# Kernel optimization log

Measured on AMD Instinct MI355X. Metric: run time of the kernel, lower is better.

Reference implementation:

```python
import jax, jax.numpy as jnp
import numpy as np

FP8_MAX = 448.0  # float8_e4m3fn max
BLOCK = 128

def act_quant(x, block_size=BLOCK):
    """Block-wise fp8 quantization along the last dim.
    Returns (q, scale): q has x.shape in float8_e4m3fn, scale has shape
    x.shape[:-1] + (K // block_size,).
    """
    *lead, K = x.shape
    nb = K // block_size
    xb = x.reshape(*lead, nb, block_size)
    amax = jnp.max(jnp.abs(xb), axis=-1)                # (..., nb)
    scale = jnp.maximum(amax / FP8_MAX, 1e-12)
    q = (xb / scale[..., None]).astype(jnp.float8_e4m3fn).reshape(x.shape)
    return q, scale

def fp8_gemm_optimized(xq, xs, kq, ks, block_size=BLOCK):
    """Dequant-scaled GEMM. xq:[M,K] fp8, xs:[M,K/bs]; kq:[K,N] fp8, ks:[K,N/bs]."""
    M, K = xq.shape
    Kk, N = kq.shape
    kb, nb = K // block_size, N // block_size
    # dequantize with per-block scales
    xd = (xq.astype(jnp.float32).reshape(M, kb, block_size)
          * xs[:, :, None]).reshape(M, K)
    kd = (kq.astype(jnp.float32).reshape(K, nb, block_size)
          * ks[:, :, None]).reshape(K, N)
    return xd @ kd

def setup_inputs() -> dict:
    key = jax.random.key(0)
    k1, k2, k3 = jax.random.split(key, 3)
    M, K, N = 16384, 4096, 4096
    x = jax.random.normal(k1, (M, K), dtype=jnp.float32)
    # lecun_normal: std = 1/sqrt(fan_in)
    kernel = jax.random.normal(k2, (K, N), dtype=jnp.float32) / jnp.sqrt(jnp.float32(K))
    bias = jnp.zeros((N,), dtype=jnp.float32)
    return {"x": x, "kernel": kernel, "bias": bias}

def reference(x, kernel, bias):
    xq, xs = act_quant(x, BLOCK)
    kq, ks = act_quant(kernel, BLOCK)
    y = fp8_gemm_optimized(xq, xs, kq, ks, BLOCK)
    return y + bias
```

## Files before the change

kernel.cpp:

```cpp
#include <hip/hip_runtime.h>


typedef __attribute__((ext_vector_type(8))) short short8;
typedef __attribute__((ext_vector_type(4))) float f32x4;
typedef unsigned short ushort_t;

__device__ __forceinline__ float fp8_round_trip(float v) {
    int p = __builtin_amdgcn_cvt_pk_fp8_f32(v, v, 0, false);
    return __builtin_amdgcn_cvt_f32_fp8(p, 0);
}

__device__ __forceinline__ ushort_t f32_to_bf16(float f) {
    union { float f; unsigned u; } un; un.f = f;
    unsigned r = un.u + 0x7fffu + ((un.u >> 16) & 1u);
    return (ushort_t)(r >> 16);
}

__device__ __forceinline__ void async16(const void* g, void* l) {
    __builtin_amdgcn_global_load_lds(
        (const __attribute__((address_space(1))) unsigned int*)g,
        (__attribute__((address_space(3))) unsigned int*)l,
        16, 0, 0);
}

__global__ __launch_bounds__(256) void quant_x_kernel(
        const float* __restrict__ x, ushort_t* __restrict__ xd) {
    size_t tid  = (size_t)blockIdx.x * 256 + threadIdx.x;
    size_t base = tid * 4;
    float4 v = *(const float4*)(x + base);
    float amax = fmaxf(fmaxf(fabsf(v.x), fabsf(v.y)),
                       fmaxf(fabsf(v.z), fabsf(v.w)));
    #pragma unroll
    for (int m = 1; m < 32; m <<= 1)
        amax = fmaxf(amax, __shfl_xor(amax, m, 64));
    float scale = fmaxf(amax / 448.0f, 1e-12f);
    ushort4 o;
    o.x = f32_to_bf16(fp8_round_trip(v.x / scale) * scale);
    o.y = f32_to_bf16(fp8_round_trip(v.y / scale) * scale);
    o.z = f32_to_bf16(fp8_round_trip(v.z / scale) * scale);
    o.w = f32_to_bf16(fp8_round_trip(v.w / scale) * scale);
    *(ushort4*)(xd + base) = o;
}

__global__ __launch_bounds__(256) void quant_w_kernel(
        const float* __restrict__ w, ushort_t* __restrict__ bt,
        int K, int N) {
    __shared__ float lds[128 * 65];
    int k0 = blockIdx.x * 64;
    int n0 = blockIdx.y * 128;
    int t = threadIdx.x;
    int wid = t >> 6, lane = t & 63;
    int half = lane >> 5, l32 = lane & 31;

    #pragma unroll
    for (int rr = 0; rr < 8; ++rr) {
        int klocal = wid * 16 + rr * 2 + half;
        int k = k0 + klocal;
        float4 v = *(const float4*)(w + (size_t)k * N + n0 + l32 * 4);
        float amax = fmaxf(fmaxf(fabsf(v.x), fabsf(v.y)),
                           fmaxf(fabsf(v.z), fabsf(v.w)));
        #pragma unroll
        for (int m = 1; m < 32; m <<= 1)
            amax = fmaxf(amax, __shfl_xor(amax, m, 64));
        float scale = fmaxf(amax / 448.0f, 1e-12f);
        int nl = l32 * 4;
        lds[(nl + 0) * 65 + klocal] = fp8_round_trip(v.x / scale) * scale;
        lds[(nl + 1) * 65 + klocal] = fp8_round_trip(v.y / scale) * scale;
        lds[(nl + 2) * 65 + klocal] = fp8_round_trip(v.z / scale) * scale;
        lds[(nl + 3) * 65 + klocal] = fp8_round_trip(v.w / scale) * scale;
    }
    __syncthreads();
    #pragma unroll
    for (int it = 0; it < 8; ++it) {
        int idx = it * 256 + t;
        int j = idx >> 4;
        int c = idx & 15;
        const float* p = &lds[j * 65 + c * 4];
        ushort4 o;
        o.x = f32_to_bf16(p[0]);
        o.y = f32_to_bf16(p[1]);
        o.z = f32_to_bf16(p[2]);
        o.w = f32_to_bf16(p[3]);
        *(ushort4*)(bt + (size_t)(n0 + j) * K + k0 + c * 4) = o;
    }
}


#define GBAR()    asm volatile("s_barrier" ::: "memory")
#define WAITL(n)  asm volatile("s_waitcnt lgkmcnt(" #n ")" ::: "memory")
#define WAITV(n)  asm volatile("s_waitcnt vmcnt(" #n ")" ::: "memory")

#define STAGE_A(h, kt, buf) do {                                             \
    const ushort_t* g_ = aSrc + (size_t)((h) * 128) * K + (size_t)(kt) * 64; \
    ushort_t* l_ = &sm[buf][0][(h) * 8192] + wid * 512;                      \
    async16(g_, l_);                                                         \
    async16(g_ + (size_t)64 * K, l_ + 4096);                                 \
} while (0)

#define STAGE_B(h, kt, buf) do {                                             \
    const ushort_t* g_ = bSrc + (size_t)((h) * 128) * K + (size_t)(kt) * 64; \
    ushort_t* l_ = &sm[buf][1][(h) * 8192] + wid * 512;                      \
    async16(g_, l_);                                                         \
    async16(g_ + (size_t)64 * K, l_ + 4096);                                 \
} while (0)

#define LDA_(dst, buf, hsel) do {                                            \
    const char* p_ = smA[buf] + aOff + (hsel) * 8192;                        \
    _Pragma("unroll") for (int m_ = 0; m_ < 4; ++m_) {                       \
        dst[m_][0] = *(const short8*)(p_ + m_ * 2048);                       \
        dst[m_][1] = *(const short8*)(p_ + m_ * 2048 + 64);                  \
    }                                                                        \
} while (0)

#define LDB_(buf, nsel) do {                                                 \
    const char* p_ = smB[buf] + bOff + (nsel) * 4096;                        \
    _Pragma("unroll") for (int n_ = 0; n_ < 2; ++n_) {                       \
        bb[n_][0] = *(const short8*)(p_ + n_ * 2048);                        \
        bb[n_][1] = *(const short8*)(p_ + n_ * 2048 + 64);                   \
    }                                                                        \
} while (0)

#define MFMAQ(AS, mb, nb) do {                                               \
    _Pragma("unroll") for (int m_ = 0; m_ < 4; ++m_)                         \
    _Pragma("unroll") for (int n_ = 0; n_ < 2; ++n_) {                       \
        acc[(mb) + m_][(nb) + n_] = __builtin_amdgcn_mfma_f32_16x16x32_bf16( \
            AS[m_][0], bb[n_][0], acc[(mb) + m_][(nb) + n_], 0, 0, 0);       \
        acc[(mb) + m_][(nb) + n_] = __builtin_amdgcn_mfma_f32_16x16x32_bf16( \
            AS[m_][1], bb[n_][1], acc[(mb) + m_][(nb) + n_], 0, 0, 0);       \
    }                                                                        \
} while (0)

#define PH_TOP()  GBAR(); WAITL(0); __builtin_amdgcn_sched_barrier(0);       \
                  __builtin_amdgcn_s_setprio(1)
#define PH_END()  __builtin_amdgcn_s_setprio(0); GBAR()

__global__ __launch_bounds__(512, 2) void gemm256_kernel(
        const ushort_t* __restrict__ A, const ushort_t* __restrict__ B,
        const float* __restrict__ bias, float* __restrict__ C,
        int M, int N, int K) {
    __shared__ ushort_t sm[2][2][16384];

    const int t = threadIdx.x;
    const int wid = t >> 6;
    const int lane = t & 63;
    const int quad = lane >> 4, l16 = lane & 15;
    const int wr = wid >> 2, wcn = wid & 3;

    const int nwg = gridDim.x;
    const int bid = blockIdx.x;
    int wg = bid;
    if ((nwg & 7) == 0) { const int cpx = nwg >> 3; wg = (bid & 7) * cpx + (bid >> 3); }
    const int nbn = N >> 8;
    const int bm = wg / nbn, bn = wg % nbn;

    const int srow = t >> 3;
    const int scol = ((((t & 7) * 16) ^ (((t >> 5) & 1) << 5)) >> 1);
    const ushort_t* aSrc = A + (size_t)(bm * 256 + srow) * K + scol;
    const ushort_t* bSrc = B + (size_t)(bn * 256 + srow) * K + scol;

    const int xr = ((l16 >> 2) & 1) << 5;
    const int tbase = l16 * 128 + ((quad * 16) ^ xr);
    const int aOff = wr * 16384 + tbase;
    const int bOff = wcn * 8192 + tbase;
    const char* smA[2] = { (const char*)sm[0][0], (const char*)sm[1][0] };
    const char* smB[2] = { (const char*)sm[0][1], (const char*)sm[1][1] };

    f32x4 acc[8][4] = {};
    short8 a0[4][2], a1[4][2], bb[2][2];

    const int NT = K >> 6;
    const int NI = NT >> 1;

    STAGE_A(0, 0, 0); STAGE_A(1, 0, 0); STAGE_B(0, 0, 0); STAGE_B(1, 0, 0);
    STAGE_A(0, 1, 1); STAGE_A(1, 1, 1); STAGE_B(0, 1, 1);
    WAITV(6); GBAR();

    for (int i = 0; i < NI; ++i) {
        const int T  = 2 * i;
        const int t1 = T + 1;
        const int t2 = (T + 2 < NT) ? T + 2 : 0;
        const int t3 = (T + 3 < NT) ? T + 3 : 0;

        LDB_(0, 0); LDA_(a0, 0, 0);
        STAGE_B(1, t1, 1);
        WAITL(8);
        PH_TOP(); MFMAQ(a0, 0, 0); PH_END();
        LDA_(a1, 0, 1);
        PH_TOP(); MFMAQ(a1, 4, 0); PH_END();
        LDB_(0, 1);
        STAGE_A(0, t2, 0);
        PH_TOP(); MFMAQ(a0, 0, 2); PH_END();
        STAGE_A(1, t2, 0);
        WAITV(4);
        GBAR(); __builtin_amdgcn_s_setprio(1); MFMAQ(a1, 4, 2); PH_END();
        LDB_(1, 0); LDA_(a0, 1, 0);
        STAGE_B(0, t2, 0);
        WAITL(8);
        PH_TOP(); MFMAQ(a0, 0, 0); PH_END();
        LDA_(a1, 1, 1);
        STAGE_B(1, t2, 0);
        PH_TOP(); MFMAQ(a1, 4, 0); PH_END();
        LDB_(1, 1);
        STAGE_A(0, t3, 1);
        PH_TOP(); MFMAQ(a0, 0, 2); PH_END();
        STAGE_A(1, t3, 1);
        STAGE_B(0, t3, 1);
        WAITV(6);
        GBAR(); __builtin_amdgcn_s_setprio(1); MFMAQ(a1, 4, 2); PH_END();
    }

    #pragma unroll
    for (int nt = 0; nt < 4; ++nt) {
        const int col = bn * 256 + wcn * 64 + nt * 16 + l16;
        const float bv = bias[col];
        #pragma unroll
        for (int mt = 0; mt < 8; ++mt) {
            const int row0 = bm * 256 + wr * 128 + mt * 16 + quad * 4;
            #pragma unroll
            for (int r = 0; r < 4; ++r)
                C[(size_t)(row0 + r) * N + col] = acc[mt][nt][r] + bv;
        }
    }
}

extern "C" void kernel_launch(void* const* d_in, const int* in_sizes, int n_in,
                              void* d_out, int out_size, void* d_ws, size_t ws_size,
                              hipStream_t stream) {
    const float* x    = (const float*)d_in[0];
    const float* w    = (const float*)d_in[1];
    const float* bias = (const float*)d_in[2];
    float* out = (float*)d_out;

    const int N = in_sizes[2];
    const int K = in_sizes[1] / N;
    const int M = in_sizes[0] / K;

    ushort_t* xd = (ushort_t*)d_ws;
    ushort_t* bt = xd + (size_t)M * K;

    quant_x_kernel<<<(size_t)M * K / 1024, 256, 0, stream>>>(x, xd);
    quant_w_kernel<<<dim3(K / 64, N / 128), 256, 0, stream>>>(w, bt, K, N);
    gemm256_kernel<<<dim3((M / 256) * (N / 256)), 512, 0, stream>>>(
        xd, bt, bias, out, M, N, K);
}
```

Baseline: 954.5 us.

## Widen LDS XOR swizzle to 8-way and double per-thread work in x quantization

The GEMM's LDS tile swizzle changes from a single-bit XOR (one 32-byte toggle) to a 3-bit row-dependent XOR over 16-byte chunks. The async global-to-LDS staging columns and the short8 fragment reads are updated to match, with the aim of removing LDS bank conflicts on the MFMA operand loads. The x quantization kernel now has each thread process two float4 groups from two 128-element blocks, halving the grid and giving more memory-level parallelism per thread. The swizzle has to stay consistent between writer and reader; a mismatch would produce wrong results, not just slower ones.

```diff
diff --git a/kernel.cpp b/kernel.cpp
--- a/kernel.cpp
+++ b/kernel.cpp
@@ -26,20 +26,34 @@
 __global__ __launch_bounds__(256) void quant_x_kernel(
         const float* __restrict__ x, ushort_t* __restrict__ xd) {
     size_t tid  = (size_t)blockIdx.x * 256 + threadIdx.x;
-    size_t base = tid * 4;
-    float4 v = *(const float4*)(x + base);
-    float amax = fmaxf(fmaxf(fabsf(v.x), fabsf(v.y)),
-                       fmaxf(fabsf(v.z), fabsf(v.w)));
-    #pragma unroll
-    for (int m = 1; m < 32; m <<= 1)
-        amax = fmaxf(amax, __shfl_xor(amax, m, 64));
-    float scale = fmaxf(amax / 448.0f, 1e-12f);
-    ushort4 o;
-    o.x = f32_to_bf16(fp8_round_trip(v.x / scale) * scale);
-    o.y = f32_to_bf16(fp8_round_trip(v.y / scale) * scale);
-    o.z = f32_to_bf16(fp8_round_trip(v.z / scale) * scale);
-    o.w = f32_to_bf16(fp8_round_trip(v.w / scale) * scale);
-    *(ushort4*)(xd + base) = o;
+    int lane = threadIdx.x & 63;
+    size_t wbase = (tid >> 6) * 512;
+    size_t i0 = wbase + (size_t)lane * 4;
+    size_t i1 = i0 + 256;
+    float4 v0 = *(const float4*)(x + i0);
+    float4 v1 = *(const float4*)(x + i1);
+    float a0 = fmaxf(fmaxf(fabsf(v0.x), fabsf(v0.y)),
+                     fmaxf(fabsf(v0.z), fabsf(v0.w)));
+    float a1 = fmaxf(fmaxf(fabsf(v1.x), fabsf(v1.y)),
+                     fmaxf(fabsf(v1.z), fabsf(v1.w)));
+    #pragma unroll
+    for (int m = 1; m < 32; m <<= 1) {
+        a0 = fmaxf(a0, __shfl_xor(a0, m, 64));
+        a1 = fmaxf(a1, __shfl_xor(a1, m, 64));
+    }
+    float s0 = fmaxf(a0 / 448.0f, 1e-12f);
+    float s1 = fmaxf(a1 / 448.0f, 1e-12f);
+    ushort4 o0, o1;
+    o0.x = f32_to_bf16(fp8_round_trip(v0.x / s0) * s0);
+    o0.y = f32_to_bf16(fp8_round_trip(v0.y / s0) * s0);
+    o0.z = f32_to_bf16(fp8_round_trip(v0.z / s0) * s0);
+    o0.w = f32_to_bf16(fp8_round_trip(v0.w / s0) * s0);
+    o1.x = f32_to_bf16(fp8_round_trip(v1.x / s1) * s1);
+    o1.y = f32_to_bf16(fp8_round_trip(v1.y / s1) * s1);
+    o1.z = f32_to_bf16(fp8_round_trip(v1.z / s1) * s1);
+    o1.w = f32_to_bf16(fp8_round_trip(v1.w / s1) * s1);
+    *(ushort4*)(xd + i0) = o0;
+    *(ushort4*)(xd + i1) = o1;
 }
 
 __global__ __launch_bounds__(256) void quant_w_kernel(
@@ -105,18 +119,18 @@
 } while (0)
 
 #define LDA_(dst, buf, hsel) do {                                            \
-    const char* p_ = smA[buf] + aOff + (hsel) * 8192;                        \
+    const char* p_ = smA[buf] + aBase + (hsel) * 8192;                       \
     _Pragma("unroll") for (int m_ = 0; m_ < 4; ++m_) {                       \
-        dst[m_][0] = *(const short8*)(p_ + m_ * 2048);                       \
-        dst[m_][1] = *(const short8*)(p_ + m_ * 2048 + 64);                  \
+        dst[m_][0] = *(const short8*)(p_ + m_ * 2048 + cs0);                 \
+        dst[m_][1] = *(const short8*)(p_ + m_ * 2048 + cs1);                 \
     }                                                                        \
 } while (0)
 
 #define LDB_(buf, nsel) do {                                                 \
-    const char* p_ = smB[buf] + bOff + (nsel) * 4096;                        \
+    const char* p_ = smB[buf] + bBase + (nsel) * 4096;                       \
     _Pragma("unroll") for (int n_ = 0; n_ < 2; ++n_) {                       \
-        bb[n_][0] = *(const short8*)(p_ + n_ * 2048);                        \
-        bb[n_][1] = *(const short8*)(p_ + n_ * 2048 + 64);                   \
+        bb[n_][0] = *(const short8*)(p_ + n_ * 2048 + cs0);                  \
+        bb[n_][1] = *(const short8*)(p_ + n_ * 2048 + cs1);                  \
     }                                                                        \
 } while (0)
 
@@ -154,14 +168,15 @@
     const int bm = wg / nbn, bn = wg % nbn;
 
     const int srow = t >> 3;
-    const int scol = ((((t & 7) * 16) ^ (((t >> 5) & 1) << 5)) >> 1);
+    const int scol = ((((t & 7) * 16) ^ (((t >> 3) & 7) << 4)) >> 1);
     const ushort_t* aSrc = A + (size_t)(bm * 256 + srow) * K + scol;
     const ushort_t* bSrc = B + (size_t)(bn * 256 + srow) * K + scol;
 
-    const int xr = ((l16 >> 2) & 1) << 5;
-    const int tbase = l16 * 128 + ((quad * 16) ^ xr);
-    const int aOff = wr * 16384 + tbase;
-    const int bOff = wcn * 8192 + tbase;
+    const int xr4 = (l16 & 7) << 4;
+    const int cs0 = (quad * 16) ^ xr4;
+    const int cs1 = (quad * 16 + 64) ^ xr4;
+    const int aBase = wr * 16384 + l16 * 128;
+    const int bBase = wcn * 8192 + l16 * 128;
     const char* smA[2] = { (const char*)sm[0][0], (const char*)sm[1][0] };
     const char* smB[2] = { (const char*)sm[0][1], (const char*)sm[1][1] };
 
@@ -238,7 +253,7 @@
     ushort_t* xd = (ushort_t*)d_ws;
     ushort_t* bt = xd + (size_t)M * K;
 
-    quant_x_kernel<<<(size_t)M * K / 1024, 256, 0, stream>>>(x, xd);
+    quant_x_kernel<<<(size_t)M * K / 2048, 256, 0, stream>>>(x, xd);
     quant_w_kernel<<<dim3(K / 64, N / 128), 256, 0, stream>>>(w, bt, K, N);
     gemm256_kernel<<<dim3((M / 256) * (N / 256)), 512, 0, stream>>>(
         xd, bt, bias, out, M, N, K);
```

Measured after the change: 925.6 us. 3.0% less time.

## Use inline-asm LDS reads with finer waitcnt splitting and wider XOR swizzle

Applied to the files above, without the earlier changes.

Replaces compiler-generated LDS fragment loads with inline ds_read_b128 asm using immediate offsets. Within each MFMA phase, waits only for the first half of the fragments before issuing MFMAs, letting the rest of the LDS reads overlap compute. It also widens the LDS swizzle from a 1-bit XOR to a 3-bit XOR on both the global-to-LDS staging and the read side, to cut bank conflicts. The partial lgkmcnt counts rely on exact issue ordering of the asm reads, so a miscount would give wrong results.

```diff
diff --git a/kernel.cpp b/kernel.cpp
--- a/kernel.cpp
+++ b/kernel.cpp
@@ -4,6 +4,7 @@
 typedef __attribute__((ext_vector_type(8))) short short8;
 typedef __attribute__((ext_vector_type(4))) float f32x4;
 typedef unsigned short ushort_t;
+typedef __attribute__((address_space(3))) const char as3ch;
 
 __device__ __forceinline__ float fp8_round_trip(float v) {
     int p = __builtin_amdgcn_cvt_pk_fp8_f32(v, v, 0, false);
@@ -89,6 +90,12 @@
 #define GBAR()    asm volatile("s_barrier" ::: "memory")
 #define WAITL(n)  asm volatile("s_waitcnt lgkmcnt(" #n ")" ::: "memory")
 #define WAITV(n)  asm volatile("s_waitcnt vmcnt(" #n ")" ::: "memory")
+#define SCHED0    __builtin_amdgcn_sched_barrier(0)
+#define SETP(n)   __builtin_amdgcn_s_setprio(n)
+#define MFMA16    __builtin_amdgcn_mfma_f32_16x16x32_bf16
+
+#define DSR(dst, base, off) \
+    asm volatile("ds_read_b128 %0, %1 offset:" #off : "=v"(dst) : "v"(base))
 
 #define STAGE_A(h, kt, buf) do {                                             \
     const ushort_t* g_ = aSrc + (size_t)((h) * 128) * K + (size_t)(kt) * 64; \
@@ -104,35 +111,36 @@
     async16(g_ + (size_t)64 * K, l_ + 4096);                                 \
 } while (0)
 
-#define LDA_(dst, buf, hsel) do {                                            \
-    const char* p_ = smA[buf] + aOff + (hsel) * 8192;                        \
-    _Pragma("unroll") for (int m_ = 0; m_ < 4; ++m_) {                       \
-        dst[m_][0] = *(const short8*)(p_ + m_ * 2048);                       \
-        dst[m_][1] = *(const short8*)(p_ + m_ * 2048 + 64);                  \
+#define PA(buf, hsel, cs) (lds3 + (buf) * 65536 + aBase + (hsel) * 8192 + (cs))
+#define PB(buf, nsel, cs) (lds3 + (buf) * 65536 + 32768 + bBase + (nsel) * 4096 + (cs))
+
+#define ISSUE_B(buf, nsel) do {                                              \
+    as3ch* p0_ = PB(buf, nsel, cs0); as3ch* p1_ = PB(buf, nsel, cs1);        \
+    DSR(bb[0][0], p0_, 0);    DSR(bb[0][1], p1_, 0);                         \
+    DSR(bb[1][0], p0_, 2048); DSR(bb[1][1], p1_, 2048);                      \
+} while (0)
+
+#define ISSUE_A(dst, buf, hsel) do {                                         \
+    as3ch* p0_ = PA(buf, hsel, cs0); as3ch* p1_ = PA(buf, hsel, cs1);        \
+    DSR(dst[0][0], p0_, 0);    DSR(dst[0][1], p1_, 0);                       \
+    DSR(dst[1][0], p0_, 2048); DSR(dst[1][1], p1_, 2048);                    \
+    DSR(dst[2][0], p0_, 4096); DSR(dst[2][1], p1_, 4096);                    \
+    DSR(dst[3][0], p0_, 6144); DSR(dst[3][1], p1_, 6144);                    \
+} while (0)
+
+#define MFMA_M(AS, mm, mb, nb) do {                                          \
+    acc[(mb)+(mm)][(nb)  ] = MFMA16(AS[mm][0], bb[0][0], acc[(mb)+(mm)][(nb)  ], 0,0,0); \
+    acc[(mb)+(mm)][(nb)+1] = MFMA16(AS[mm][0], bb[1][0], acc[(mb)+(mm)][(nb)+1], 0,0,0); \
+    acc[(mb)+(mm)][(nb)  ] = MFMA16(AS[mm][1], bb[0][1], acc[(mb)+(mm)][(nb)  ], 0,0,0); \
+    acc[(mb)+(mm)][(nb)+1] = MFMA16(AS[mm][1], bb[1][1], acc[(mb)+(mm)][(nb)+1], 0,0,0); \
+} while (0)
+
+#define MFMA_N(AS, n_, mb, nb) do {                                          \
+    _Pragma("unroll") for (int mm_ = 0; mm_ < 4; ++mm_) {                    \
+        acc[(mb)+mm_][(nb)+(n_)] = MFMA16(AS[mm_][0], bb[n_][0], acc[(mb)+mm_][(nb)+(n_)], 0,0,0); \
+        acc[(mb)+mm_][(nb)+(n_)] = MFMA16(AS[mm_][1], bb[n_][1], acc[(mb)+mm_][(nb)+(n_)], 0,0,0); \
     }                                                                        \
 } while (0)
-
-#define LDB_(buf, nsel) do {                                                 \
-    const char* p_ = smB[buf] + bOff + (nsel) * 4096;                        \
-    _Pragma("unroll") for (int n_ = 0; n_ < 2; ++n_) {                       \
-        bb[n_][0] = *(const short8*)(p_ + n_ * 2048);                        \
-        bb[n_][1] = *(const short8*)(p_ + n_ * 2048 + 64);                   \
-    }                                                                        \
-} while (0)
-
-#define MFMAQ(AS, mb, nb) do {                                               \
-    _Pragma("unroll") for (int m_ = 0; m_ < 4; ++m_)                         \
-    _Pragma("unroll") for (int n_ = 0; n_ < 2; ++n_) {                       \
-        acc[(mb) + m_][(nb) + n_] = __builtin_amdgcn_mfma_f32_16x16x32_bf16( \
-            AS[m_][0], bb[n_][0], acc[(mb) + m_][(nb) + n_], 0, 0, 0);       \
-        acc[(mb) + m_][(nb) + n_] = __builtin_amdgcn_mfma_f32_16x16x32_bf16( \
-            AS[m_][1], bb[n_][1], acc[(mb) + m_][(nb) + n_], 0, 0, 0);       \
-    }                                                                        \
-} while (0)
-
-#define PH_TOP()  GBAR(); WAITL(0); __builtin_amdgcn_sched_barrier(0);       \
-                  __builtin_amdgcn_s_setprio(1)
-#define PH_END()  __builtin_amdgcn_s_setprio(0); GBAR()
 
 __global__ __launch_bounds__(512, 2) void gemm256_kernel(
         const ushort_t* __restrict__ A, const ushort_t* __restrict__ B,
@@ -154,16 +162,16 @@
     const int bm = wg / nbn, bn = wg % nbn;
 
     const int srow = t >> 3;
-    const int scol = ((((t & 7) * 16) ^ (((t >> 5) & 1) << 5)) >> 1);
+    const int scol = ((((t & 7) * 16) ^ (((t >> 3) & 7) << 4)) >> 1);
     const ushort_t* aSrc = A + (size_t)(bm * 256 + srow) * K + scol;
     const ushort_t* bSrc = B + (size_t)(bn * 256 + srow) * K + scol;
 
-    const int xr = ((l16 >> 2) & 1) << 5;
-    const int tbase = l16 * 128 + ((quad * 16) ^ xr);
-    const int aOff = wr * 16384 + tbase;
-    const int bOff = wcn * 8192 + tbase;
-    const char* smA[2] = { (const char*)sm[0][0], (const char*)sm[1][0] };
-    const char* smB[2] = { (const char*)sm[0][1], (const char*)sm[1][1] };
+    const int xr4 = (l16 & 7) << 4;
+    const int cs0 = (quad * 16) ^ xr4;
+    const int cs1 = (quad * 16 + 64) ^ xr4;
+    const int aBase = wr * 16384 + l16 * 128;
+    const int bBase = wcn * 8192 + l16 * 128;
+    as3ch* lds3 = (as3ch*)sm;
 
     f32x4 acc[8][4] = {};
     short8 a0[4][2], a1[4][2], bb[2][2];
@@ -181,32 +189,64 @@
         const int t2 = (T + 2 < NT) ? T + 2 : 0;
         const int t3 = (T + 3 < NT) ? T + 3 : 0;
 
-        LDB_(0, 0); LDA_(a0, 0, 0);
+        ISSUE_B(0, 0); ISSUE_A(a0, 0, 0);
         STAGE_B(1, t1, 1);
-        WAITL(8);
-        PH_TOP(); MFMAQ(a0, 0, 0); PH_END();
-        LDA_(a1, 0, 1);
-        PH_TOP(); MFMAQ(a1, 4, 0); PH_END();
-        LDB_(0, 1);
+        GBAR();
+        WAITL(4); SCHED0; SETP(1);
+        MFMA_M(a0, 0, 0, 0); MFMA_M(a0, 1, 0, 0);
+        WAITL(0); SCHED0;
+        MFMA_M(a0, 2, 0, 0); MFMA_M(a0, 3, 0, 0);
+        SETP(0); GBAR();
+        ISSUE_A(a1, 0, 1);
+        GBAR();
+        WAITL(4); SCHED0; SETP(1);
+        MFMA_M(a1, 0, 4, 0); MFMA_M(a1, 1, 4, 0);
+        WAITL(0); SCHED0;
+        MFMA_M(a1, 2, 4, 0); MFMA_M(a1, 3, 4, 0);
+        SETP(0); GBAR();
+        ISSUE_B(0, 1);
         STAGE_A(0, t2, 0);
-        PH_TOP(); MFMAQ(a0, 0, 2); PH_END();
+        GBAR();
+        WAITL(2); SCHED0; SETP(1);
+        MFMA_N(a0, 0, 0, 2);
+        WAITL(0); SCHED0;
+        MFMA_N(a0, 1, 0, 2);
+        SETP(0); GBAR();
         STAGE_A(1, t2, 0);
         WAITV(4);
-        GBAR(); __builtin_amdgcn_s_setprio(1); MFMAQ(a1, 4, 2); PH_END();
-        LDB_(1, 0); LDA_(a0, 1, 0);
+        GBAR(); SETP(1);
+        MFMA_N(a1, 0, 4, 2); MFMA_N(a1, 1, 4, 2);
+        SETP(0); GBAR();
+        ISSUE_B(1, 0); ISSUE_A(a0, 1, 0);
         STAGE_B(0, t2, 0);
-        WAITL(8);
-        PH_TOP(); MFMAQ(a0, 0, 0); PH_END();
-        LDA_(a1, 1, 1);
+        GBAR();
+        WAITL(4); SCHED0; SETP(1);
+        MFMA_M(a0, 0, 0, 0); MFMA_M(a0, 1, 0, 0);
+        WAITL(0); SCHED0;
+        MFMA_M(a0, 2, 0, 0); MFMA_M(a0, 3, 0, 0);
+        SETP(0); GBAR();
+        ISSUE_A(a1, 1, 1);
         STAGE_B(1, t2, 0);
-        PH_TOP(); MFMAQ(a1, 4, 0); PH_END();
-        LDB_(1, 1);
+        GBAR();
+        WAITL(4); SCHED0; SETP(1);
+        MFMA_M(a1, 0, 4, 0); MFMA_M(a1, 1, 4, 0);
+        WAITL(0); SCHED0;
+        MFMA_M(a1, 2, 4, 0); MFMA_M(a1, 3, 4, 0);
+        SETP(0); GBAR();
+        ISSUE_B(1, 1);
         STAGE_A(0, t3, 1);
-        PH_TOP(); MFMAQ(a0, 0, 2); PH_END();
+        GBAR();
+        WAITL(2); SCHED0; SETP(1);
+        MFMA_N(a0, 0, 0, 2);
+        WAITL(0); SCHED0;
+        MFMA_N(a0, 1, 0, 2);
+        SETP(0); GBAR();
         STAGE_A(1, t3, 1);
         STAGE_B(0, t3, 1);
         WAITV(6);
-        GBAR(); __builtin_amdgcn_s_setprio(1); MFMAQ(a1, 4, 2); PH_END();
+        GBAR(); SETP(1);
+        MFMA_N(a1, 0, 4, 2); MFMA_N(a1, 1, 4, 2);
+        SETP(0); GBAR();
     }
 
     #pragma unroll
```

After: 905.2 us. -5.2%, faster.
